# Optimization experiments

Measured on AMD Instinct MI355X. Metric: run time of the kernel, lower is better.

The kernel has to match this reference:

```python
import jax, jax.numpy as jnp
import numpy as np

WINDOW = 128
BACKWARD = 1
FORWARD = 0

def look_around(x, pad_value):
    # x: [b, windows, window_size, ...]; pad window axis and gather shifted windows
    w = x.shape[1]
    pads = [(0, 0), (BACKWARD, FORWARD)] + [(0, 0)] * (x.ndim - 2)
    p = jnp.pad(x, pads, constant_values=pad_value)
    return jnp.concatenate([p[:, i:i + w] for i in range(BACKWARD + FORWARD + 1)], axis=2)

def setup_inputs() -> dict:
    key = jax.random.key(0)
    ks = jax.random.split(key, 5)
    shp = (2, 16, 4096, 64)
    names = ['q', 'k', 'q_rot', 'k_rot', 'v']
    inp = {n: jax.random.normal(ks[i], shp, dtype=jnp.float32) for i, n in enumerate(names)}
    inp['states'] = 0
    inp['inferring_states'] = 0
    return inp

def reference(q, k, q_rot, k_rot, v, states, inferring_states):
    shape = q.shape
    merge = lambda t: t.reshape(-1, t.shape[-2], t.shape[-1])
    q, k, q_rot, k_rot, v = map(merge, (q, k, q_rot, k_rot, v))
    b, t, e = q.shape
    windows = t // WINDOW
    ticker = jnp.arange(t, dtype=q.dtype)[None, :]
    b_t = ticker.reshape(1, windows, WINDOW)
    bucket = lambda x: x.reshape(b, windows, WINDOW, e)
    bq, bk, bq_rot, bk_rot, bv = map(bucket, (q, k, q_rot, k_rot, v))
    bk = look_around(bk, 0.0)
    bk_rot = look_around(bk_rot, 0.0)
    bv = look_around(bv, 0.0)
    bq_t = b_t
    bq_k = look_around(b_t, -1.0)
    scale = e ** (-0.5)
    dots = jnp.einsum('bwie,bwje->bwij', bq, bk) * scale
    dots_rot = jnp.einsum('bwie,bwje->bwij', bq_rot, bk_rot) * scale
    mask_value = -jnp.finfo(dots.dtype).max
    causal_mask = bq_t[:, :, :, None] < bq_k[:, :, None, :]
    pad_mask = bq_k[:, :, None, :] == -1
    mask = causal_mask | pad_mask
    dots = jnp.where(mask, mask_value, dots)
    dots_rot = jnp.where(mask, mask_value, dots_rot)
    attn = jax.nn.softmax(dots + dots_rot, axis=-1)
    out = jnp.einsum('bwij,bwje->bwie', attn, bv)
    return out.reshape(shape)
```

## Files before the change

### kernel.cpp

```cpp
#include <hip/hip_runtime.h>
#include <stdint.h>

#define T 4096
#define E 64
#define NBH 32
#define NWIN 32
#define LDKS 128
#define LDVS 64
#define KK_ELEMS (64*LDKS)
#define VT_ELEMS (64*LDVS)
#define BUF_ELEMS (KK_ELEMS+VT_ELEMS)
#define SMEM_BYTES (2*BUF_ELEMS*2)

typedef __attribute__((ext_vector_type(8))) short short8;
typedef __attribute__((ext_vector_type(4))) short short4v;
typedef __attribute__((ext_vector_type(4))) float f32x4;

__device__ __forceinline__ short f2bf(float x) {
  unsigned u = __float_as_uint(x);
  u += 0x7fffu + ((u >> 16) & 1u);
  return (short)(u >> 16);
}

__device__ __forceinline__ unsigned cvtpk(float lo, float hi) {
  unsigned r;
  asm("v_cvt_pk_bf16_f32 %0, %1, %2" : "=v"(r) : "v"(lo), "v"(hi));
  return r;
}

__device__ __forceinline__ void block_sync_lds() {
  asm volatile("s_waitcnt lgkmcnt(0)" ::: "memory");
  __builtin_amdgcn_s_barrier();
  asm volatile("" ::: "memory");
}

struct SubStage { float4 sk[4]; float sv[8]; };

__device__ __forceinline__ void sub_issue(SubStage& st,
    const float* __restrict__ k, const float* __restrict__ kr,
    const float* __restrict__ v, size_t rowbase, int tid, int wid, int lane) {
#pragma unroll
  for (int m = 0; m < 2; ++m) {
    const float* src = m ? kr : k;
#pragma unroll
    for (int it = 0; it < 2; ++it) {
      int idx = it * 512 + tid;
      st.sk[m * 2 + it] = *(const float4*)(src + (rowbase + (idx >> 4)) * E + (idx & 15) * 4);
    }
  }
  const float* vp = v + (rowbase + wid * 8) * E + lane;
#pragma unroll
  for (int i = 0; i < 8; ++i) st.sv[i] = vp[(size_t)i * E];
}

__device__ __forceinline__ void sub_commit(const SubStage& st,
    short* __restrict__ KK, short* __restrict__ Vt, int tid, int wid, int lane) {
#pragma unroll
  for (int m = 0; m < 2; ++m)
#pragma unroll
    for (int it = 0; it < 2; ++it) {
      int idx = it * 512 + tid;
      int row = idx >> 4;
      int chunk = m * 8 + ((idx & 15) >> 1);
      float4 f = st.sk[m * 2 + it];
      short4v h = { f2bf(f.x), f2bf(f.y), f2bf(f.z), f2bf(f.w) };
      *(short4v*)(KK + row * LDKS + ((chunk ^ (row & 15)) << 3) + (idx & 1) * 4) = h;
    }
#pragma unroll
  for (int rq = 0; rq < 2; ++rq) {
    short4v h = { f2bf(st.sv[rq*4+0]), f2bf(st.sv[rq*4+1]),
                  f2bf(st.sv[rq*4+2]), f2bf(st.sv[rq*4+3]) };
    *(short4v*)(Vt + lane * LDVS + ((wid ^ (lane & 7)) << 3) + rq * 4) = h;
  }
}

__device__ __forceinline__ void q_issue(float4* sq,
    const float* __restrict__ q, const float* __restrict__ qr,
    size_t rbase, int w, int wid, int li, int lg) {
  const size_t qrow = rbase + (size_t)w * 128 + wid * 16 + li;
#pragma unroll
  for (int kt = 0; kt < 4; ++kt) {
    const float* sp = (kt < 2 ? q : qr) + qrow * E + (kt & 1) * 32 + lg * 8;
    sq[kt * 2 + 0] = *(const float4*)sp;
    sq[kt * 2 + 1] = *(const float4*)(sp + 4);
  }
}

__device__ __forceinline__ void q_commit(const float4* sq, short8* aF) {
#pragma unroll
  for (int kt = 0; kt < 4; ++kt) {
    float4 f0 = sq[kt * 2], f1 = sq[kt * 2 + 1];
    short8 a;
    a[0]=f2bf(f0.x*0.125f); a[1]=f2bf(f0.y*0.125f); a[2]=f2bf(f0.z*0.125f); a[3]=f2bf(f0.w*0.125f);
    a[4]=f2bf(f1.x*0.125f); a[5]=f2bf(f1.y*0.125f); a[6]=f2bf(f1.z*0.125f); a[7]=f2bf(f1.w*0.125f);
    aF[kt] = a;
  }
}

__global__ __launch_bounds__(512, 4)
void la_attn(const float* __restrict__ qg, const float* __restrict__ kg,
             const float* __restrict__ qrg, const float* __restrict__ krg,
             const float* __restrict__ vg, float* __restrict__ outg) {
  extern __shared__ short smem[];

  const int lid = blockIdx.y * NWIN + blockIdx.x;
  const int wl  = (lid & 7) * 128 + (lid >> 3);
  const int win = wl & (NWIN - 1), bh = wl >> 5;

  const int tid = threadIdx.x;
  const int wid = tid >> 6, lane = tid & 63;
  const int li = lane & 15, lg = lane >> 4;
  const size_t rbase = (size_t)bh * T;
  const int q_i = wid * 16 + li;

  short8 aF[4];
  SubStage st;

  const int s0 = (win == 0) ? 2 : 0;
#define KROW(s) (rbase + (size_t)(win * 128 + ((s) - 2) * 64))

  {
    SubStage stA;
    float4 sq[8];
    sub_issue(stA, kg, krg, vg, KROW(s0), tid, wid, lane);
    q_issue(sq, qg, qrg, rbase, win, wid, li, lg);
    sub_commit(stA, smem, smem + KK_ELEMS, tid, wid, lane);
    q_commit(sq, aF);
    if (s0 + 1 < 4) sub_issue(st, kg, krg, vg, KROW(s0 + 1), tid, wid, lane);
  }
  block_sync_lds();

  float m = -1e30f, l = 0.f;
  f32x4 O[4] = {{0,0,0,0},{0,0,0,0},{0,0,0,0},{0,0,0,0}};

  for (int s = s0; s < 4; ++s) {
    const int cur = (s - s0) & 1;
    short* KKc = smem + cur * BUF_ELEMS;
    short* Vtc = KKc + KK_ELEMS;

    if (s + 1 < 4) {
      sub_commit(st, smem + (cur ^ 1) * BUF_ELEMS,
                 smem + (cur ^ 1) * BUF_ELEMS + KK_ELEMS, tid, wid, lane);
      if (s + 2 < 4) sub_issue(st, kg, krg, vg, KROW(s + 2), tid, wid, lane);
      asm volatile("" ::: "memory");
    }

    f32x4 p[4];
#pragma unroll
    for (int ct = 0; ct < 4; ++ct) {
      f32x4 acc = {0.f, 0.f, 0.f, 0.f};
      const int row = ct * 16 + li;
#pragma unroll
      for (int kt = 0; kt < 4; ++kt) {
        const short* kb = KKc + row * LDKS + (((kt * 4 + lg) ^ li) << 3);
        acc = __builtin_amdgcn_mfma_f32_16x16x32_bf16(*(const short8*)kb, aF[kt], acc, 0, 0, 0);
      }
      p[ct] = acc;
    }

    if (s >= 2) {
      const int joff = (s - 2) * 64 + lg * 4;
#pragma unroll
      for (int ct = 0; ct < 4; ++ct)
#pragma unroll
        for (int r = 0; r < 4; ++r)
          if (joff + ct * 16 + r > q_i) p[ct][r] = -1e30f;
    }
    float mx = -1e30f;
#pragma unroll
    for (int ct = 0; ct < 4; ++ct)
#pragma unroll
      for (int r = 0; r < 4; ++r) mx = fmaxf(mx, p[ct][r]);
    mx = fmaxf(mx, __shfl_xor(mx, 16));
    mx = fmaxf(mx, __shfl_xor(mx, 32));
    const float mn = fmaxf(m, mx);
    const float f = __expf(m - mn);
    float sm = 0.f;
#pragma unroll
    for (int ct = 0; ct < 4; ++ct)
#pragma unroll
      for (int r = 0; r < 4; ++r) {
        float e = __expf(p[ct][r] - mn);
        p[ct][r] = e;
        sm += e;
      }
    sm += __shfl_xor(sm, 16);
    sm += __shfl_xor(sm, 32);
    l = l * f + sm;
    m = mn;
#pragma unroll
    for (int nt = 0; nt < 4; ++nt)
#pragma unroll
      for (int r = 0; r < 4; ++r) O[nt][r] *= f;

    unsigned W0[4], W1[4];
#pragma unroll
    for (int ct = 0; ct < 4; ++ct) {
      W0[ct] = cvtpk(p[ct][0], p[ct][1]);
      W1[ct] = cvtpk(p[ct][2], p[ct][3]);
    }

    const bool lowhalf = (lg < 2);
    const bool sendR = (lg == 0) | (lg == 3);
#pragma unroll
    for (int kt = 0; kt < 2; ++kt) {
      const int cA = kt * 2, cB = cA + 1;
      unsigned P0 = lowhalf ? W0[cB] : W0[cA];
      unsigned P1 = lowhalf ? W1[cB] : W1[cA];
      unsigned R0 = __shfl_xor(P0, 32);
      unsigned R1 = __shfl_xor(P1, 32);
      unsigned L0 = lowhalf ? W0[cA] : W0[cB];
      unsigned L1 = lowhalf ? W1[cA] : W1[cB];
      unsigned S0 = sendR ? R0 : L0;
      unsigned S1 = sendR ? R1 : L1;
      unsigned T0 = __shfl_xor(S0, 16);
      unsigned T1 = __shfl_xor(S1, 16);
      unsigned F0 = (lg == 0) ? L0 : ((lg == 2) ? R0 : T0);
      unsigned F1 = (lg == 0) ? L1 : ((lg == 2) ? R1 : T1);
      unsigned G0 = (lg == 1) ? R0 : ((lg == 3) ? L0 : T0);
      unsigned G1 = (lg == 1) ? R1 : ((lg == 3) ? L1 : T1);
      union { unsigned u[4]; short8 s; } bu;
      bu.u[0] = F0; bu.u[1] = F1; bu.u[2] = G0; bu.u[3] = G1;
      const short8 bP = bu.s;
#pragma unroll
      for (int nt = 0; nt < 4; ++nt) {
        const short* vb = Vtc + (nt * 16 + li) * LDVS + (((kt * 4 + lg) ^ (li & 7)) << 3);
        O[nt] = __builtin_amdgcn_mfma_f32_16x16x32_bf16(*(const short8*)vb, bP, O[nt], 0, 0, 0);
      }
    }

    block_sync_lds();
  }

  const float linv = 1.f / l;
  float* op = outg + (rbase + (size_t)win * 128 + wid * 16 + li) * E + lg * 4;
#pragma unroll
  for (int nt = 0; nt < 4; ++nt) {
    float4 o = { O[nt][0] * linv, O[nt][1] * linv, O[nt][2] * linv, O[nt][3] * linv };
    *(float4*)(op + nt * 16) = o;
  }
#undef KROW
}

extern "C" void kernel_launch(void* const* d_in, const int* in_sizes, int n_in,
                              void* d_out, int out_size, void* d_ws, size_t ws_size,
                              hipStream_t stream) {
  const float* q  = (const float*)d_in[0];
  const float* k  = (const float*)d_in[1];
  const float* qr = (const float*)d_in[2];
  const float* kr = (const float*)d_in[3];
  const float* v  = (const float*)d_in[4];
  float* out = (float*)d_out;
  la_attn<<<dim3(NWIN, NBH), 512, SMEM_BYTES, stream>>>(q, k, qr, kr, v, out);
}
```

Before: 201.3 us.

## Process two adjacent windows per block, sharing K/V chunk loads across them

Each block now handles a strip of two consecutive windows. Four waves serve each window, and each wave owns 32 query rows split into two 16-row tiles. K/V chunks stream through six stages covering both windows, so the overlapping middle chunks are loaded and converted once instead of twice. Half the waves sit idle in stages outside their window. Softmax now uses exp2 with log2e folded into the Q scale, and the bf16 conversion uses the hardware pack instruction. This cuts global traffic and conversion work, at the cost of more registers per thread and lower per-stage MFMA utilization.

```diff
diff --git a/kernel.cpp b/kernel.cpp
--- a/kernel.cpp
+++ b/kernel.cpp
@@ -5,22 +5,18 @@
 #define E 64
 #define NBH 32
 #define NWIN 32
+#define NSTRIP 16
 #define LDKS 128
 #define LDVS 64
 #define KK_ELEMS (64*LDKS)
 #define VT_ELEMS (64*LDVS)
 #define BUF_ELEMS (KK_ELEMS+VT_ELEMS)
 #define SMEM_BYTES (2*BUF_ELEMS*2)
+#define QSCALE 0.180336880f
 
 typedef __attribute__((ext_vector_type(8))) short short8;
 typedef __attribute__((ext_vector_type(4))) short short4v;
 typedef __attribute__((ext_vector_type(4))) float f32x4;
-
-__device__ __forceinline__ short f2bf(float x) {
-  unsigned u = __float_as_uint(x);
-  u += 0x7fffu + ((u >> 16) & 1u);
-  return (short)(u >> 16);
-}
 
 __device__ __forceinline__ unsigned cvtpk(float lo, float hi) {
   unsigned r;
@@ -28,6 +24,13 @@
   return r;
 }
 
+__device__ __forceinline__ short8 pack8s(float4 f0, float4 f1, float s) {
+  union { unsigned u[4]; short8 s8; } r;
+  r.u[0] = cvtpk(f0.x*s, f0.y*s); r.u[1] = cvtpk(f0.z*s, f0.w*s);
+  r.u[2] = cvtpk(f1.x*s, f1.y*s); r.u[3] = cvtpk(f1.z*s, f1.w*s);
+  return r.s8;
+}
+
 __device__ __forceinline__ void block_sync_lds() {
   asm volatile("s_waitcnt lgkmcnt(0)" ::: "memory");
   __builtin_amdgcn_s_barrier();
@@ -38,7 +41,7 @@
 
 __device__ __forceinline__ void sub_issue(SubStage& st,
     const float* __restrict__ k, const float* __restrict__ kr,
-    const float* __restrict__ v, size_t rowbase, int tid, int wid, int lane) {
+    const float* __restrict__ v, size_t rowbase, int tid, int wv, int lane) {
 #pragma unroll
   for (int m = 0; m < 2; ++m) {
     const float* src = m ? kr : k;
@@ -48,13 +51,13 @@
       st.sk[m * 2 + it] = *(const float4*)(src + (rowbase + (idx >> 4)) * E + (idx & 15) * 4);
     }
   }
-  const float* vp = v + (rowbase + wid * 8) * E + lane;
+  const float* vp = v + (rowbase + wv * 8) * E + lane;
 #pragma unroll
   for (int i = 0; i < 8; ++i) st.sv[i] = vp[(size_t)i * E];
 }
 
 __device__ __forceinline__ void sub_commit(const SubStage& st,
-    short* __restrict__ KK, short* __restrict__ Vt, int tid, int wid, int lane) {
+    short* __restrict__ KK, short* __restrict__ Vt, int tid, int wv, int lane) {
 #pragma unroll
   for (int m = 0; m < 2; ++m)
 #pragma unroll
@@ -63,38 +66,41 @@
       int row = idx >> 4;
       int chunk = m * 8 + ((idx & 15) >> 1);
       float4 f = st.sk[m * 2 + it];
-      short4v h = { f2bf(f.x), f2bf(f.y), f2bf(f.z), f2bf(f.w) };
-      *(short4v*)(KK + row * LDKS + ((chunk ^ (row & 15)) << 3) + (idx & 1) * 4) = h;
+      union { unsigned u[2]; short4v s; } h;
+      h.u[0] = cvtpk(f.x, f.y); h.u[1] = cvtpk(f.z, f.w);
+      *(short4v*)(KK + row * LDKS + ((chunk ^ (row & 15)) << 3) + (idx & 1) * 4) = h.s;
     }
 #pragma unroll
   for (int rq = 0; rq < 2; ++rq) {
-    short4v h = { f2bf(st.sv[rq*4+0]), f2bf(st.sv[rq*4+1]),
-                  f2bf(st.sv[rq*4+2]), f2bf(st.sv[rq*4+3]) };
-    *(short4v*)(Vt + lane * LDVS + ((wid ^ (lane & 7)) << 3) + rq * 4) = h;
-  }
-}
-
-__device__ __forceinline__ void q_issue(float4* sq,
-    const float* __restrict__ q, const float* __restrict__ qr,
-    size_t rbase, int w, int wid, int li, int lg) {
-  const size_t qrow = rbase + (size_t)w * 128 + wid * 16 + li;
-#pragma unroll
-  for (int kt = 0; kt < 4; ++kt) {
-    const float* sp = (kt < 2 ? q : qr) + qrow * E + (kt & 1) * 32 + lg * 8;
-    sq[kt * 2 + 0] = *(const float4*)sp;
-    sq[kt * 2 + 1] = *(const float4*)(sp + 4);
-  }
-}
-
-__device__ __forceinline__ void q_commit(const float4* sq, short8* aF) {
-#pragma unroll
-  for (int kt = 0; kt < 4; ++kt) {
-    float4 f0 = sq[kt * 2], f1 = sq[kt * 2 + 1];
-    short8 a;
-    a[0]=f2bf(f0.x*0.125f); a[1]=f2bf(f0.y*0.125f); a[2]=f2bf(f0.z*0.125f); a[3]=f2bf(f0.w*0.125f);
-    a[4]=f2bf(f1.x*0.125f); a[5]=f2bf(f1.y*0.125f); a[6]=f2bf(f1.z*0.125f); a[7]=f2bf(f1.w*0.125f);
-    aF[kt] = a;
-  }
+    union { unsigned u[2]; short4v s; } h;
+    h.u[0] = cvtpk(st.sv[rq*4+0], st.sv[rq*4+1]);
+    h.u[1] = cvtpk(st.sv[rq*4+2], st.sv[rq*4+3]);
+    *(short4v*)(Vt + lane * LDVS + ((wv ^ (lane & 7)) << 3) + rq * 4) = h.s;
+  }
+}
+
+__device__ __forceinline__ short8 pv_bfrag(const unsigned* W0, const unsigned* W1,
+                                           int kt, int lg) {
+  const bool lowhalf = (lg < 2);
+  const bool sendR = (lg == 0) | (lg == 3);
+  const int cA = kt * 2, cB = cA + 1;
+  unsigned P0 = lowhalf ? W0[cB] : W0[cA];
+  unsigned P1 = lowhalf ? W1[cB] : W1[cA];
+  unsigned R0 = __shfl_xor(P0, 32);
+  unsigned R1 = __shfl_xor(P1, 32);
+  unsigned L0 = lowhalf ? W0[cA] : W0[cB];
+  unsigned L1 = lowhalf ? W1[cA] : W1[cB];
+  unsigned S0 = sendR ? R0 : L0;
+  unsigned S1 = sendR ? R1 : L1;
+  unsigned T0 = __shfl_xor(S0, 16);
+  unsigned T1 = __shfl_xor(S1, 16);
+  unsigned F0 = (lg == 0) ? L0 : ((lg == 2) ? R0 : T0);
+  unsigned F1 = (lg == 0) ? L1 : ((lg == 2) ? R1 : T1);
+  unsigned G0 = (lg == 1) ? R0 : ((lg == 3) ? L0 : T0);
+  unsigned G1 = (lg == 1) ? R1 : ((lg == 3) ? L1 : T1);
+  union { unsigned u[4]; short8 s; } bu;
+  bu.u[0] = F0; bu.u[1] = F1; bu.u[2] = G0; bu.u[3] = G1;
+  return bu.s;
 }
 
 __global__ __launch_bounds__(512, 4)
@@ -103,141 +109,156 @@
              const float* __restrict__ vg, float* __restrict__ outg) {
   extern __shared__ short smem[];
 
-  const int lid = blockIdx.y * NWIN + blockIdx.x;
-  const int wl  = (lid & 7) * 128 + (lid >> 3);
-  const int win = wl & (NWIN - 1), bh = wl >> 5;
+  const int lid = blockIdx.y * NSTRIP + blockIdx.x;
+  const int wl  = (lid & 7) * 64 + (lid >> 3);
+  const int strip = wl & (NSTRIP - 1), bh = wl >> 4;
 
   const int tid = threadIdx.x;
-  const int wid = tid >> 6, lane = tid & 63;
+  const int wv = tid >> 6, lane = tid & 63;
   const int li = lane & 15, lg = lane >> 4;
+  const int dw = wv >> 2;
+  const int win = strip * 2 + dw;
+  const int tb = (wv & 3) * 32;
   const size_t rbase = (size_t)bh * T;
-  const int q_i = wid * 16 + li;
-
-  short8 aF[4];
+
+  short8 aF[2][4];
+#pragma unroll
+  for (int qt = 0; qt < 2; ++qt) {
+    const size_t qrow = rbase + (size_t)win * 128 + tb + qt * 16 + li;
+#pragma unroll
+    for (int kt = 0; kt < 4; ++kt) {
+      const float* sp = (kt < 2 ? qg : qrg) + qrow * E + (kt & 1) * 32 + lg * 8;
+      aF[qt][kt] = pack8s(*(const float4*)sp, *(const float4*)(sp + 4), QSCALE);
+    }
+  }
+
   SubStage st;
-
-  const int s0 = (win == 0) ? 2 : 0;
-#define KROW(s) (rbase + (size_t)(win * 128 + ((s) - 2) * 64))
+  const int s_start = (strip == 0) ? 2 : 0;
+#define KROW(s) (rbase + (size_t)(strip * 256 + (s) * 64 - 128))
 
   {
     SubStage stA;
-    float4 sq[8];
-    sub_issue(stA, kg, krg, vg, KROW(s0), tid, wid, lane);
-    q_issue(sq, qg, qrg, rbase, win, wid, li, lg);
-    sub_commit(stA, smem, smem + KK_ELEMS, tid, wid, lane);
-    q_commit(sq, aF);
-    if (s0 + 1 < 4) sub_issue(st, kg, krg, vg, KROW(s0 + 1), tid, wid, lane);
+    sub_issue(stA, kg, krg, vg, KROW(s_start), tid, wv, lane);
+    sub_commit(stA, smem, smem + KK_ELEMS, tid, wv, lane);
+    sub_issue(st, kg, krg, vg, KROW(s_start + 1), tid, wv, lane);
   }
   block_sync_lds();
 
-  float m = -1e30f, l = 0.f;
-  f32x4 O[4] = {{0,0,0,0},{0,0,0,0},{0,0,0,0},{0,0,0,0}};
-
-  for (int s = s0; s < 4; ++s) {
-    const int cur = (s - s0) & 1;
+  float m[2] = {-1e30f, -1e30f}, l[2] = {0.f, 0.f};
+  f32x4 O[2][4];
+#pragma unroll
+  for (int qt = 0; qt < 2; ++qt)
+#pragma unroll
+    for (int nt = 0; nt < 4; ++nt) O[qt][nt] = f32x4{0.f, 0.f, 0.f, 0.f};
+
+  for (int s = s_start; s < 6; ++s) {
+    const int cur = (s - s_start) & 1;
     short* KKc = smem + cur * BUF_ELEMS;
     short* Vtc = KKc + KK_ELEMS;
 
-    if (s + 1 < 4) {
+    if (s + 1 < 6) {
       sub_commit(st, smem + (cur ^ 1) * BUF_ELEMS,
-                 smem + (cur ^ 1) * BUF_ELEMS + KK_ELEMS, tid, wid, lane);
-      if (s + 2 < 4) sub_issue(st, kg, krg, vg, KROW(s + 2), tid, wid, lane);
+                 smem + (cur ^ 1) * BUF_ELEMS + KK_ELEMS, tid, wv, lane);
+      if (s + 2 < 6) sub_issue(st, kg, krg, vg, KROW(s + 2), tid, wv, lane);
       asm volatile("" ::: "memory");
     }
 
-    f32x4 p[4];
-#pragma unroll
-    for (int ct = 0; ct < 4; ++ct) {
-      f32x4 acc = {0.f, 0.f, 0.f, 0.f};
-      const int row = ct * 16 + li;
-#pragma unroll
-      for (int kt = 0; kt < 4; ++kt) {
-        const short* kb = KKc + row * LDKS + (((kt * 4 + lg) ^ li) << 3);
-        acc = __builtin_amdgcn_mfma_f32_16x16x32_bf16(*(const short8*)kb, aF[kt], acc, 0, 0, 0);
-      }
-      p[ct] = acc;
-    }
-
-    if (s >= 2) {
-      const int joff = (s - 2) * 64 + lg * 4;
-#pragma unroll
-      for (int ct = 0; ct < 4; ++ct)
-#pragma unroll
-        for (int r = 0; r < 4; ++r)
-          if (joff + ct * 16 + r > q_i) p[ct][r] = -1e30f;
-    }
-    float mx = -1e30f;
-#pragma unroll
-    for (int ct = 0; ct < 4; ++ct)
-#pragma unroll
-      for (int r = 0; r < 4; ++r) mx = fmaxf(mx, p[ct][r]);
-    mx = fmaxf(mx, __shfl_xor(mx, 16));
-    mx = fmaxf(mx, __shfl_xor(mx, 32));
-    const float mn = fmaxf(m, mx);
-    const float f = __expf(m - mn);
-    float sm = 0.f;
-#pragma unroll
-    for (int ct = 0; ct < 4; ++ct)
-#pragma unroll
-      for (int r = 0; r < 4; ++r) {
-        float e = __expf(p[ct][r] - mn);
-        p[ct][r] = e;
-        sm += e;
-      }
-    sm += __shfl_xor(sm, 16);
-    sm += __shfl_xor(sm, 32);
-    l = l * f + sm;
-    m = mn;
-#pragma unroll
-    for (int nt = 0; nt < 4; ++nt)
-#pragma unroll
-      for (int r = 0; r < 4; ++r) O[nt][r] *= f;
-
-    unsigned W0[4], W1[4];
-#pragma unroll
-    for (int ct = 0; ct < 4; ++ct) {
-      W0[ct] = cvtpk(p[ct][0], p[ct][1]);
-      W1[ct] = cvtpk(p[ct][2], p[ct][3]);
-    }
-
-    const bool lowhalf = (lg < 2);
-    const bool sendR = (lg == 0) | (lg == 3);
-#pragma unroll
-    for (int kt = 0; kt < 2; ++kt) {
-      const int cA = kt * 2, cB = cA + 1;
-      unsigned P0 = lowhalf ? W0[cB] : W0[cA];
-      unsigned P1 = lowhalf ? W1[cB] : W1[cA];
-      unsigned R0 = __shfl_xor(P0, 32);
-      unsigned R1 = __shfl_xor(P1, 32);
-      unsigned L0 = lowhalf ? W0[cA] : W0[cB];
-      unsigned L1 = lowhalf ? W1[cA] : W1[cB];
-      unsigned S0 = sendR ? R0 : L0;
-      unsigned S1 = sendR ? R1 : L1;
-      unsigned T0 = __shfl_xor(S0, 16);
-      unsigned T1 = __shfl_xor(S1, 16);
-      unsigned F0 = (lg == 0) ? L0 : ((lg == 2) ? R0 : T0);
-      unsigned F1 = (lg == 0) ? L1 : ((lg == 2) ? R1 : T1);
-      unsigned G0 = (lg == 1) ? R0 : ((lg == 3) ? L0 : T0);
-      unsigned G1 = (lg == 1) ? R1 : ((lg == 3) ? L1 : T1);
-      union { unsigned u[4]; short8 s; } bu;
-      bu.u[0] = F0; bu.u[1] = F1; bu.u[2] = G0; bu.u[3] = G1;
-      const short8 bP = bu.s;
-#pragma unroll
-      for (int nt = 0; nt < 4; ++nt) {
-        const short* vb = Vtc + (nt * 16 + li) * LDVS + (((kt * 4 + lg) ^ (li & 7)) << 3);
-        O[nt] = __builtin_amdgcn_mfma_f32_16x16x32_bf16(*(const short8*)vb, bP, O[nt], 0, 0, 0);
+    const int rel = s - 2 * dw;
+    if (rel >= 0 && rel < 4) {
+      f32x4 p[2][4];
+#pragma unroll
+      for (int qt = 0; qt < 2; ++qt)
+#pragma unroll
+        for (int ct = 0; ct < 4; ++ct) p[qt][ct] = f32x4{0.f, 0.f, 0.f, 0.f};
+#pragma unroll
+      for (int ct = 0; ct < 4; ++ct) {
+        const int row = ct * 16 + li;
+#pragma unroll
+        for (int kt = 0; kt < 4; ++kt) {
+          const short8 kb = *(const short8*)(KKc + row * LDKS + (((kt * 4 + lg) ^ li) << 3));
+          p[0][ct] = __builtin_amdgcn_mfma_f32_16x16x32_bf16(kb, aF[0][kt], p[0][ct], 0, 0, 0);
+          p[1][ct] = __builtin_amdgcn_mfma_f32_16x16x32_bf16(kb, aF[1][kt], p[1][ct], 0, 0, 0);
+        }
+      }
+
+      if (rel >= 2) {
+        const int kpos = (rel - 2) * 64 + lg * 4;
+#pragma unroll
+        for (int qt = 0; qt < 2; ++qt) {
+          const int q_i = tb + qt * 16 + li;
+#pragma unroll
+          for (int ct = 0; ct < 4; ++ct)
+#pragma unroll
+            for (int r = 0; r < 4; ++r)
+              if (kpos + ct * 16 + r > q_i) p[qt][ct][r] = -1e30f;
+        }
+      }
+
+      unsigned W0[2][4], W1[2][4];
+#pragma unroll
+      for (int qt = 0; qt < 2; ++qt) {
+        float mx = -1e30f;
+#pragma unroll
+        for (int ct = 0; ct < 4; ++ct)
+#pragma unroll
+          for (int r = 0; r < 4; ++r) mx = fmaxf(mx, p[qt][ct][r]);
+        mx = fmaxf(mx, __shfl_xor(mx, 16));
+        mx = fmaxf(mx, __shfl_xor(mx, 32));
+        const float mn = fmaxf(m[qt], mx);
+        const float f = exp2f(m[qt] - mn);
+        float sm = 0.f;
+#pragma unroll
+        for (int ct = 0; ct < 4; ++ct)
+#pragma unroll
+          for (int r = 0; r < 4; ++r) {
+            float e = exp2f(p[qt][ct][r] - mn);
+            p[qt][ct][r] = e;
+            sm += e;
+          }
+        sm += __shfl_xor(sm, 16);
+        sm += __shfl_xor(sm, 32);
+        l[qt] = l[qt] * f + sm;
+        m[qt] = mn;
+#pragma unroll
+        for (int nt = 0; nt < 4; ++nt)
+#pragma unroll
+          for (int r = 0; r < 4; ++r) O[qt][nt][r] *= f;
+#pragma unroll
+        for (int ct = 0; ct < 4; ++ct) {
+          W0[qt][ct] = cvtpk(p[qt][ct][0], p[qt][ct][1]);
+          W1[qt][ct] = cvtpk(p[qt][ct][2], p[qt][ct][3]);
+        }
+      }
+
+#pragma unroll
+      for (int kt = 0; kt < 2; ++kt) {
+        short8 vA[4];
+#pragma unroll
+        for (int nt = 0; nt < 4; ++nt)
+          vA[nt] = *(const short8*)(Vtc + (nt * 16 + li) * LDVS + (((kt * 4 + lg) ^ (li & 7)) << 3));
+#pragma unroll
+        for (int qt = 0; qt < 2; ++qt) {
+          const short8 bP = pv_bfrag(W0[qt], W1[qt], kt, lg);
+#pragma unroll
+          for (int nt = 0; nt < 4; ++nt)
+            O[qt][nt] = __builtin_amdgcn_mfma_f32_16x16x32_bf16(vA[nt], bP, O[qt][nt], 0, 0, 0);
+        }
       }
     }
 
     block_sync_lds();
   }
 
-  const float linv = 1.f / l;
-  float* op = outg + (rbase + (size_t)win * 128 + wid * 16 + li) * E + lg * 4;
-#pragma unroll
-  for (int nt = 0; nt < 4; ++nt) {
-    float4 o = { O[nt][0] * linv, O[nt][1] * linv, O[nt][2] * linv, O[nt][3] * linv };
-    *(float4*)(op + nt * 16) = o;
+#pragma unroll
+  for (int qt = 0; qt < 2; ++qt) {
+    const float linv = 1.f / l[qt];
+    float* op = outg + (rbase + (size_t)win * 128 + tb + qt * 16 + li) * E + lg * 4;
+#pragma unroll
+    for (int nt = 0; nt < 4; ++nt) {
+      float4 o = { O[qt][nt][0] * linv, O[qt][nt][1] * linv,
+                   O[qt][nt][2] * linv, O[qt][nt][3] * linv };
+      *(float4*)(op + nt * 16) = o;
+    }
   }
 #undef KROW
 }
@@ -251,5 +272,5 @@
   const float* kr = (const float*)d_in[3];
   const float* v  = (const float*)d_in[4];
   float* out = (float*)d_out;
-  la_attn<<<dim3(NWIN, NBH), 512, SMEM_BYTES, stream>>>(q, k, qr, kr, v, out);
-}
+  la_attn<<<dim3(NSTRIP, NBH), 512, SMEM_BYTES, stream>>>(q, k, qr, kr, v, out);
+}
```

Measured after the change: 299.5 us. 1.49x slower.
